# Kernel tuning notes

Measured on AMD Instinct MI355X. Metric: run time of the kernel, lower is better.

Reference implementation:

```python
import jax, jax.numpy as jnp
import numpy as np

B, L, D, H = 2, 2048, 1024, 16
DK = D // H
EPS = 1e-6


def setup_inputs() -> dict:
    key = jax.random.key(0)
    ks = jax.random.split(key, 8)
    s = 0.02
    return {
        "key": jax.random.normal(ks[0], (B, L, D), jnp.float32),
        "value": jax.random.normal(ks[1], (B, L, D), jnp.float32),
        "query": jax.random.normal(ks[2], (B, L, D), jnp.float32),
        "mask": jax.random.randint(ks[3], (B, L, L), 0, 2).astype(bool),
        "W_k": jax.random.normal(ks[4], (D, D), jnp.float32) * s,
        "W_v": jax.random.normal(ks[5], (D, D), jnp.float32) * s,
        "W_q": jax.random.normal(ks[6], (D, D), jnp.float32) * s,
        "ln_g": jnp.ones((D,), jnp.float32),
        "ln_b": jnp.zeros((D,), jnp.float32),
    }


def _mha(key, value, query, mask, W_k, W_v, W_q, ln_g, ln_b):
    b, l, d = key.shape
    # projections (bias=False), split into heads: [b, h, l, dk]
    def proj(x, W):
        return (x @ W).reshape(b, -1, H, DK).transpose(0, 2, 1, 3)
    k_up, v_up, q_up = proj(key, W_k), proj(value, W_v), proj(query, W_q)
    # scores [b, h, q, k]
    scores = jnp.einsum("bhqd,bhkd->bhqk", q_up, k_up) / jnp.sqrt(jnp.asarray(DK, scores_dtype(q_up)))
    scores = jnp.where(mask[:, None, :, :], -1e9, scores)
    attn = jax.nn.softmax(scores, axis=-1)  # dropout = identity (eval mode)
    out = jnp.einsum("bhqk,bhkd->bhqd", attn, v_up)
    out = out.transpose(0, 2, 1, 3).reshape(b, -1, d)
    res = out + query  # res_dropout = identity
    mu = jnp.mean(res, axis=-1, keepdims=True)
    var = jnp.var(res, axis=-1, keepdims=True)
    normed = (res - mu) * jax.lax.rsqrt(var + EPS) * ln_g + ln_b
    return normed, attn.reshape(b * H, attn.shape[2], attn.shape[3])


def scores_dtype(x):
    return x.dtype


def reference(key, value, query, mask, W_k, W_v, W_q, ln_g, ln_b):
    return _mha(key, value, query, mask, W_k, W_v, W_q, ln_g, ln_b)
```

## Files before the change

### kernel.cpp

```cpp
#include <hip/hip_runtime.h>
#include <math.h>

#define BATCH 2
#define SEQ   2048
#define DMODEL 1024
#define NHEAD 16
#define DK    64
#define EPS   1e-6f

typedef unsigned short ushort_t;
typedef __attribute__((ext_vector_type(8))) __bf16 bf16x8;
typedef __attribute__((ext_vector_type(4))) float f32x4;
typedef __attribute__((ext_vector_type(4))) unsigned int uivec4;

union B8U { uivec4 u; bf16x8 v; };

__device__ __forceinline__ ushort_t f2b(float x) {
    union { float f; unsigned int u; } c; c.f = x;
    unsigned int r = (c.u + 0x7fffu + ((c.u >> 16) & 1u)) >> 16;
    return (ushort_t)r;
}
__device__ __forceinline__ float b2f(ushort_t b) {
    union { unsigned int u; float f; } c; c.u = ((unsigned int)b) << 16;
    return c.f;
}
__device__ __forceinline__ bf16x8 ld_frag_lds(const ushort_t* p) {
    B8U t; t.u = *reinterpret_cast<const uivec4*>(p); return t.v;
}
__device__ __forceinline__ bf16x8 ld_frag_glb(const ushort_t* p) {
    B8U t; t.u = *reinterpret_cast<const uivec4*>(p); return t.v;
}
#define MFMA16(a, b, c) __builtin_amdgcn_mfma_f32_16x16x32_bf16((a), (b), (c), 0, 0, 0)

__global__ __launch_bounds__(256) void mask_to_bits(const int* __restrict__ mask,
                                                    unsigned int* __restrict__ bits) {
    const size_t widx = (size_t)blockIdx.x * 256 + threadIdx.x;
    const int4* src = reinterpret_cast<const int4*>(mask + widx * 32);
    unsigned int wv = 0;
    #pragma unroll
    for (int i = 0; i < 8; ++i) {
        int4 v = src[i];
        wv |= (v.x ? 1u : 0u) << (i * 4 + 0);
        wv |= (v.y ? 1u : 0u) << (i * 4 + 1);
        wv |= (v.z ? 1u : 0u) << (i * 4 + 2);
        wv |= (v.w ? 1u : 0u) << (i * 4 + 3);
    }
    bits[widx] = wv;
}

#define AST 40
#define BST 40
__global__ __launch_bounds__(256) void gemm_proj3(const float* __restrict__ X0,
                                                  const float* __restrict__ X1,
                                                  const float* __restrict__ X2,
                                                  const float* __restrict__ W0,
                                                  const float* __restrict__ W1,
                                                  const float* __restrict__ W2,
                                                  ushort_t* __restrict__ Y0,
                                                  ushort_t* __restrict__ Y1,
                                                  ushort_t* __restrict__ Y2) {
    __shared__ __align__(16) ushort_t As[128 * AST];
    __shared__ __align__(16) ushort_t Bt[128 * BST];
    const int z = blockIdx.z;
    const float* X = (z == 0) ? X0 : (z == 1) ? X1 : X2;
    const float* W = (z == 0) ? W0 : (z == 1) ? W1 : W2;
    ushort_t*    Y = (z == 0) ? Y0 : (z == 1) ? Y1 : Y2;

    const int t = threadIdx.x;
    const int bm = blockIdx.y * 128;
    const int bn = blockIdx.x * 128;
    const int w = t >> 6, lane = t & 63;
    const int ln16 = lane & 15, quad = lane >> 4;
    const int wr = w >> 1, wc = w & 1;

    f32x4 acc[4][4] = {};

    for (int k0 = 0; k0 < DMODEL; k0 += 32) {
        {
            const int m = t >> 1, half = t & 1;
            const float* src = X + (size_t)(bm + m) * DMODEL + k0 + half * 16;
            ushort_t* dst = &As[m * AST + half * 16];
            #pragma unroll
            for (int i = 0; i < 16; ++i) dst[i] = f2b(src[i]);
        }
        {
            const int kk = t >> 3, n0 = (t & 7) * 16;
            const float* src = W + (size_t)(k0 + kk) * DMODEL + bn + n0;
            #pragma unroll
            for (int i = 0; i < 16; ++i) Bt[(n0 + i) * BST + kk] = f2b(src[i]);
        }
        __syncthreads();
        bf16x8 af[4], bfr[4];
        #pragma unroll
        for (int rt = 0; rt < 4; ++rt)
            af[rt] = ld_frag_lds(&As[(wr * 64 + rt * 16 + ln16) * AST + quad * 8]);
        #pragma unroll
        for (int ct = 0; ct < 4; ++ct)
            bfr[ct] = ld_frag_lds(&Bt[(wc * 64 + ct * 16 + ln16) * BST + quad * 8]);
        #pragma unroll
        for (int rt = 0; rt < 4; ++rt)
            #pragma unroll
            for (int ct = 0; ct < 4; ++ct)
                acc[rt][ct] = MFMA16(af[rt], bfr[ct], acc[rt][ct]);
        __syncthreads();
    }
    #pragma unroll
    for (int rt = 0; rt < 4; ++rt) {
        #pragma unroll
        for (int ct = 0; ct < 4; ++ct) {
            #pragma unroll
            for (int r = 0; r < 4; ++r) {
                int row = bm + wr * 64 + rt * 16 + quad * 4 + r;
                int col = bn + wc * 64 + ct * 16 + ln16;
                Y[(size_t)row * DMODEL + col] = f2b(acc[rt][ct][r]);
            }
        }
    }
}

__global__ __launch_bounds__(256) void transpose_v(const ushort_t* __restrict__ v_up,
                                                   ushort_t* __restrict__ v_t) {
    __shared__ ushort_t tile[64][68];
    const int t = threadIdx.x;
    const int s0 = blockIdx.x * 64;
    const int bh = blockIdx.y;
    const int b = bh >> 4, h = bh & 15;
    {
        const int r = t >> 2, c0 = (t & 3) * 16;
        const ushort_t* src = v_up + ((size_t)b * SEQ + s0 + r) * DMODEL + h * DK + c0;
        #pragma unroll
        for (int i = 0; i < 16; ++i) tile[r][c0 + i] = src[i];
    }
    __syncthreads();
    {
        const int c = t >> 2, r0 = (t & 3) * 16;
        ushort_t* dst = v_t + ((size_t)bh * DK + c) * SEQ + s0 + r0;
        #pragma unroll
        for (int i = 0; i < 16; ++i) dst[i] = tile[r0 + i][c];
    }
}

#define PST 264
__global__ __launch_bounds__(512, 4) void attn_fused(const ushort_t* __restrict__ q_up,
                                                     const ushort_t* __restrict__ k_up,
                                                     const ushort_t* __restrict__ v_t,
                                                     const unsigned int* __restrict__ mbits,
                                                     float* __restrict__ attn,
                                                     float* __restrict__ o_ws) {
    __shared__ __align__(16) ushort_t Pb[32 * PST];
    __shared__ float psum[8][32];
    __shared__ float inv_s[32];

    const int t = threadIdx.x;
    const int w = t >> 6, lane = t & 63;
    const int ln16 = lane & 15, quad = lane >> 4;
    const int q0 = blockIdx.x * 32;
    const int bh = blockIdx.y;
    const int b = bh >> 4, h = bh & 15;

    bf16x8 aq[2][2];
    #pragma unroll
    for (int rt = 0; rt < 2; ++rt)
        #pragma unroll
        for (int ks = 0; ks < 2; ++ks)
            aq[rt][ks] = ld_frag_glb(
                &q_up[((size_t)b * SEQ + q0 + rt * 16 + ln16) * DMODEL + h * DK + ks * 32 + quad * 8]);

    const unsigned int* mrow = mbits + ((size_t)b * SEQ + q0) * (SEQ / 32);
    const ushort_t* kbase = &k_up[(size_t)b * SEQ * DMODEL + h * DK + quad * 8];

    float rs[2][4] = {};
    for (int i = 0; i < 16; ++i) {
        const int kt = (i * 8 + w) * 16;
        bf16x8 bk0 = ld_frag_glb(kbase + (size_t)(kt + ln16) * DMODEL);
        bf16x8 bk1 = ld_frag_glb(kbase + (size_t)(kt + ln16) * DMODEL + 32);
        const int wi = kt >> 5;
        const int bsh = (kt & 16) + ln16;
        #pragma unroll
        for (int rt = 0; rt < 2; ++rt) {
            f32x4 c = {0.f, 0.f, 0.f, 0.f};
            c = MFMA16(aq[rt][0], bk0, c);
            c = MFMA16(aq[rt][1], bk1, c);
            #pragma unroll
            for (int r = 0; r < 4; ++r) {
                const int row = rt * 16 + quad * 4 + r;
                const unsigned int mw = mrow[(size_t)row * (SEQ / 32) + wi];
                const float p = ((mw >> bsh) & 1u) ? 0.f : __expf(c[r] * 0.125f);
                rs[rt][r] += p;
            }
        }
    }
    #pragma unroll
    for (int rt = 0; rt < 2; ++rt)
        #pragma unroll
        for (int r = 0; r < 4; ++r) {
            float v = rs[rt][r];
            v += __shfl_xor(v, 1);
            v += __shfl_xor(v, 2);
            v += __shfl_xor(v, 4);
            v += __shfl_xor(v, 8);
            rs[rt][r] = v;
        }
    if (ln16 == 0) {
        #pragma unroll
        for (int rt = 0; rt < 2; ++rt)
            #pragma unroll
            for (int r = 0; r < 4; ++r)
                psum[w][rt * 16 + quad * 4 + r] = rs[rt][r];
    }
    __syncthreads();
    if (t < 32) {
        float s = 0.f;
        #pragma unroll
        for (int j = 0; j < 8; ++j) s += psum[j][t];
        inv_s[t] = 1.f / s;
    }
    __syncthreads();
    float invr[2][4];
    #pragma unroll
    for (int rt = 0; rt < 2; ++rt)
        #pragma unroll
        for (int r = 0; r < 4; ++r)
            invr[rt][r] = inv_s[rt * 16 + quad * 4 + r];

    const int prt = w >> 2, pct = w & 3;
    f32x4 acc = {0.f, 0.f, 0.f, 0.f};
    const ushort_t* vbase = &v_t[((size_t)bh * DK + pct * 16 + ln16) * SEQ + quad * 8];
    float* abase = attn + ((size_t)bh * SEQ + q0) * SEQ;
    const ushort_t* prow = &Pb[(prt * 16 + ln16) * PST + quad * 8];

    for (int kb = 0; kb < SEQ; kb += 256) {
        #pragma unroll
        for (int tl = 0; tl < 2; ++tl) {
            const int kt = kb + (w * 2 + tl) * 16;
            bf16x8 bk0 = ld_frag_glb(kbase + (size_t)(kt + ln16) * DMODEL);
            bf16x8 bk1 = ld_frag_glb(kbase + (size_t)(kt + ln16) * DMODEL + 32);
            const int wi = kt >> 5;
            const int bsh = (kt & 16) + ln16;
            #pragma unroll
            for (int rt = 0; rt < 2; ++rt) {
                f32x4 c = {0.f, 0.f, 0.f, 0.f};
                c = MFMA16(aq[rt][0], bk0, c);
                c = MFMA16(aq[rt][1], bk1, c);
                #pragma unroll
                for (int r = 0; r < 4; ++r) {
                    const int row = rt * 16 + quad * 4 + r;
                    const unsigned int mw = mrow[(size_t)row * (SEQ / 32) + wi];
                    const float p = ((mw >> bsh) & 1u) ? 0.f : __expf(c[r] * 0.125f);
                    const float pn = p * invr[rt][r];
                    __builtin_nontemporal_store(pn, &abase[(size_t)row * SEQ + kt + ln16]);
                    Pb[row * PST + (kt - kb) + ln16] = f2b(pn);
                }
            }
        }
        __syncthreads();
        #pragma unroll
        for (int k0 = 0; k0 < 256; k0 += 32) {
            bf16x8 a  = ld_frag_lds(prow + k0);
            bf16x8 vb = ld_frag_glb(vbase + kb + k0);
            acc = MFMA16(a, vb, acc);
        }
        __syncthreads();
    }
    #pragma unroll
    for (int r = 0; r < 4; ++r) {
        const int row = q0 + prt * 16 + quad * 4 + r;
        const int col = h * DK + pct * 16 + ln16;
        o_ws[((size_t)b * SEQ + row) * DMODEL + col] = acc[r];
    }
}

__global__ __launch_bounds__(256) void ln_kernel(const float* __restrict__ O,
                                                 const float* __restrict__ Qin,
                                                 const float* __restrict__ g,
                                                 const float* __restrict__ bt,
                                                 float* __restrict__ out) {
    __shared__ float sm[256];
    const int tid = threadIdx.x;
    const size_t base = (size_t)blockIdx.x * DMODEL;
    float v[4];
    float s = 0.f, s2 = 0.f;
    #pragma unroll
    for (int i = 0; i < 4; ++i) {
        int d = tid + i * 256;
        float x = O[base + d] + Qin[base + d];
        v[i] = x;
        s += x;
        s2 += x * x;
    }
    sm[tid] = s; __syncthreads();
    for (int st = 128; st > 0; st >>= 1) {
        if (tid < st) sm[tid] += sm[tid + st];
        __syncthreads();
    }
    s = sm[0]; __syncthreads();
    sm[tid] = s2; __syncthreads();
    for (int st = 128; st > 0; st >>= 1) {
        if (tid < st) sm[tid] += sm[tid + st];
        __syncthreads();
    }
    s2 = sm[0];
    const float mu = s * (1.0f / DMODEL);
    const float var = s2 * (1.0f / DMODEL) - mu * mu;
    const float r = rsqrtf(var + EPS);
    #pragma unroll
    for (int i = 0; i < 4; ++i) {
        int d = tid + i * 256;
        out[base + d] = (v[i] - mu) * r * g[d] + bt[d];
    }
}

extern "C" void kernel_launch(void* const* d_in, const int* in_sizes, int n_in,
                              void* d_out, int out_size, void* d_ws, size_t ws_size,
                              hipStream_t stream) {
    const float* key   = (const float*)d_in[0];
    const float* value = (const float*)d_in[1];
    const float* query = (const float*)d_in[2];
    const int*   mask  = (const int*)  d_in[3];
    const float* W_k   = (const float*)d_in[4];
    const float* W_v   = (const float*)d_in[5];
    const float* W_q   = (const float*)d_in[6];
    const float* ln_g  = (const float*)d_in[7];
    const float* ln_b  = (const float*)d_in[8];

    float* out      = (float*)d_out;
    float* attn_out = out + (size_t)BATCH * SEQ * DMODEL;

    const size_t NPROJ = (size_t)BATCH * SEQ * DMODEL;
    ushort_t* k_up = (ushort_t*)d_ws;
    ushort_t* v_up = k_up + NPROJ;
    ushort_t* q_up = v_up + NPROJ;
    ushort_t* v_t  = q_up + NPROJ;
    float*    o_ws = (float*)(v_t + NPROJ);
    unsigned int* mbits = (unsigned int*)(o_ws + NPROJ);

    const int nwords = BATCH * SEQ * (SEQ / 32);
    mask_to_bits<<<nwords / 256, 256, 0, stream>>>(mask, mbits);

    dim3 gproj(DMODEL / 128, (BATCH * SEQ) / 128, 3);
    gemm_proj3<<<gproj, 256, 0, stream>>>(key, value, query, W_k, W_v, W_q, k_up, v_up, q_up);

    dim3 gtr(SEQ / 64, BATCH * NHEAD);
    transpose_v<<<gtr, 256, 0, stream>>>(v_up, v_t);

    dim3 gat(SEQ / 32, BATCH * NHEAD);
    attn_fused<<<gat, 512, 0, stream>>>(q_up, k_up, v_t, mbits, attn_out, o_ws);

    ln_kernel<<<BATCH * SEQ, 256, 0, stream>>>(o_ws, query, ln_g, ln_b, out);
}
```

Before: 919.5 us.

## Pre-convert inputs and weights to bf16, load GEMM tiles via global_load_lds

Adds separate kernels that convert the three fp32 activations to bf16 and transpose-convert the weights to bf16 N-major. The projection GEMM then streams tiles straight into LDS with global_load_lds instead of per-element fp32 loads, conversion and strided transposed LDS stores. It also raises wave priority around MFMA sections in the GEMM and attention kernels. In exchange it adds extra kernel launches, more workspace traffic, and an unpadded LDS layout that may cause bank conflicts.

```diff
diff --git a/kernel.cpp b/kernel.cpp
--- a/kernel.cpp
+++ b/kernel.cpp
@@ -30,6 +30,12 @@
 __device__ __forceinline__ bf16x8 ld_frag_glb(const ushort_t* p) {
     B8U t; t.u = *reinterpret_cast<const uivec4*>(p); return t.v;
 }
+__device__ __forceinline__ void gload_lds16(const ushort_t* g, ushort_t* l) {
+    __builtin_amdgcn_global_load_lds(
+        (const __attribute__((address_space(1))) unsigned int*)g,
+        (__attribute__((address_space(3))) unsigned int*)l,
+        16, 0, 0);
+}
 #define MFMA16(a, b, c) __builtin_amdgcn_mfma_f32_16x16x32_bf16((a), (b), (c), 0, 0, 0)
 
 __global__ __launch_bounds__(256) void mask_to_bits(const int* __restrict__ mask,
@@ -48,23 +54,67 @@
     bits[widx] = wv;
 }
 
-#define AST 40
-#define BST 40
-__global__ __launch_bounds__(256) void gemm_proj3(const float* __restrict__ X0,
+__global__ __launch_bounds__(256) void cvt_bf16x3(const float* __restrict__ X0,
                                                   const float* __restrict__ X1,
                                                   const float* __restrict__ X2,
-                                                  const float* __restrict__ W0,
-                                                  const float* __restrict__ W1,
-                                                  const float* __restrict__ W2,
                                                   ushort_t* __restrict__ Y0,
                                                   ushort_t* __restrict__ Y1,
                                                   ushort_t* __restrict__ Y2) {
-    __shared__ __align__(16) ushort_t As[128 * AST];
-    __shared__ __align__(16) ushort_t Bt[128 * BST];
+    const int z = blockIdx.y;
+    const float* X = (z == 0) ? X0 : (z == 1) ? X1 : X2;
+    ushort_t*    Y = (z == 0) ? Y0 : (z == 1) ? Y1 : Y2;
+    const size_t i = ((size_t)blockIdx.x * 256 + threadIdx.x) * 8;
+    float4 a = *reinterpret_cast<const float4*>(X + i);
+    float4 b = *reinterpret_cast<const float4*>(X + i + 4);
+    ushort_t o[8];
+    o[0] = f2b(a.x); o[1] = f2b(a.y); o[2] = f2b(a.z); o[3] = f2b(a.w);
+    o[4] = f2b(b.x); o[5] = f2b(b.y); o[6] = f2b(b.z); o[7] = f2b(b.w);
+    *reinterpret_cast<uivec4*>(Y + i) = *reinterpret_cast<const uivec4*>(o);
+}
+
+__global__ __launch_bounds__(256) void transpose_w3(const float* __restrict__ W0,
+                                                    const float* __restrict__ W1,
+                                                    const float* __restrict__ W2,
+                                                    ushort_t* __restrict__ T0,
+                                                    ushort_t* __restrict__ T1,
+                                                    ushort_t* __restrict__ T2) {
+    __shared__ ushort_t tile[64][68];
     const int z = blockIdx.z;
-    const float* X = (z == 0) ? X0 : (z == 1) ? X1 : X2;
     const float* W = (z == 0) ? W0 : (z == 1) ? W1 : W2;
-    ushort_t*    Y = (z == 0) ? Y0 : (z == 1) ? Y1 : Y2;
+    ushort_t*    T = (z == 0) ? T0 : (z == 1) ? T1 : T2;
+    const int k0 = blockIdx.x * 64;
+    const int n0 = blockIdx.y * 64;
+    const int t = threadIdx.x;
+    {
+        const int r = t >> 2, c0 = (t & 3) * 16;
+        const float* src = W + (size_t)(k0 + r) * DMODEL + n0 + c0;
+        #pragma unroll
+        for (int i = 0; i < 16; ++i) tile[r][c0 + i] = f2b(src[i]);
+    }
+    __syncthreads();
+    {
+        const int c = t >> 2, r0 = (t & 3) * 16;
+        ushort_t* dst = T + (size_t)(n0 + c) * DMODEL + k0 + r0;
+        #pragma unroll
+        for (int i = 0; i < 16; ++i) dst[i] = tile[r0 + i][c];
+    }
+}
+
+__global__ __launch_bounds__(256) void gemm_proj3(const ushort_t* __restrict__ Xb0,
+                                                  const ushort_t* __restrict__ Xb1,
+                                                  const ushort_t* __restrict__ Xb2,
+                                                  const ushort_t* __restrict__ Wt0,
+                                                  const ushort_t* __restrict__ Wt1,
+                                                  const ushort_t* __restrict__ Wt2,
+                                                  ushort_t* __restrict__ Y0,
+                                                  ushort_t* __restrict__ Y1,
+                                                  ushort_t* __restrict__ Y2) {
+    __shared__ __align__(16) ushort_t As[128 * 32];
+    __shared__ __align__(16) ushort_t Bs[128 * 32];
+    const int z = blockIdx.z;
+    const ushort_t* Xb = (z == 0) ? Xb0 : (z == 1) ? Xb1 : Xb2;
+    const ushort_t* Wt = (z == 0) ? Wt0 : (z == 1) ? Wt1 : Wt2;
+    ushort_t*       Y  = (z == 0) ? Y0  : (z == 1) ? Y1  : Y2;
 
     const int t = threadIdx.x;
     const int bm = blockIdx.y * 128;
@@ -73,35 +123,34 @@
     const int ln16 = lane & 15, quad = lane >> 4;
     const int wr = w >> 1, wc = w & 1;
 
+    const int srow = lane >> 2;
+    const int selem = (lane & 3) * 8;
+
     f32x4 acc[4][4] = {};
 
     for (int k0 = 0; k0 < DMODEL; k0 += 32) {
-        {
-            const int m = t >> 1, half = t & 1;
-            const float* src = X + (size_t)(bm + m) * DMODEL + k0 + half * 16;
-            ushort_t* dst = &As[m * AST + half * 16];
-            #pragma unroll
-            for (int i = 0; i < 16; ++i) dst[i] = f2b(src[i]);
-        }
-        {
-            const int kk = t >> 3, n0 = (t & 7) * 16;
-            const float* src = W + (size_t)(k0 + kk) * DMODEL + bn + n0;
-            #pragma unroll
-            for (int i = 0; i < 16; ++i) Bt[(n0 + i) * BST + kk] = f2b(src[i]);
+        #pragma unroll
+        for (int j = 0; j < 2; ++j) {
+            const int g = w * 2 + j;
+            const int m = g * 16 + srow;
+            gload_lds16(Xb + (size_t)(bm + m) * DMODEL + k0 + selem, &As[g * 512]);
+            gload_lds16(Wt + (size_t)(bn + m) * DMODEL + k0 + selem, &Bs[g * 512]);
         }
         __syncthreads();
         bf16x8 af[4], bfr[4];
         #pragma unroll
         for (int rt = 0; rt < 4; ++rt)
-            af[rt] = ld_frag_lds(&As[(wr * 64 + rt * 16 + ln16) * AST + quad * 8]);
+            af[rt] = ld_frag_lds(&As[(wr * 64 + rt * 16 + ln16) * 32 + quad * 8]);
         #pragma unroll
         for (int ct = 0; ct < 4; ++ct)
-            bfr[ct] = ld_frag_lds(&Bt[(wc * 64 + ct * 16 + ln16) * BST + quad * 8]);
+            bfr[ct] = ld_frag_lds(&Bs[(wc * 64 + ct * 16 + ln16) * 32 + quad * 8]);
+        __builtin_amdgcn_s_setprio(1);
         #pragma unroll
         for (int rt = 0; rt < 4; ++rt)
             #pragma unroll
             for (int ct = 0; ct < 4; ++ct)
                 acc[rt][ct] = MFMA16(af[rt], bfr[ct], acc[rt][ct]);
+        __builtin_amdgcn_s_setprio(0);
         __syncthreads();
     }
     #pragma unroll
@@ -179,8 +228,10 @@
         #pragma unroll
         for (int rt = 0; rt < 2; ++rt) {
             f32x4 c = {0.f, 0.f, 0.f, 0.f};
+            __builtin_amdgcn_s_setprio(1);
             c = MFMA16(aq[rt][0], bk0, c);
             c = MFMA16(aq[rt][1], bk1, c);
+            __builtin_amdgcn_s_setprio(0);
             #pragma unroll
             for (int r = 0; r < 4; ++r) {
                 const int row = rt * 16 + quad * 4 + r;
@@ -240,8 +291,10 @@
             #pragma unroll
             for (int rt = 0; rt < 2; ++rt) {
                 f32x4 c = {0.f, 0.f, 0.f, 0.f};
+                __builtin_amdgcn_s_setprio(1);
                 c = MFMA16(aq[rt][0], bk0, c);
                 c = MFMA16(aq[rt][1], bk1, c);
+                __builtin_amdgcn_s_setprio(0);
                 #pragma unroll
                 for (int r = 0; r < 4; ++r) {
                     const int row = rt * 16 + quad * 4 + r;
@@ -254,12 +307,14 @@
             }
         }
         __syncthreads();
+        __builtin_amdgcn_s_setprio(1);
         #pragma unroll
         for (int k0 = 0; k0 < 256; k0 += 32) {
             bf16x8 a  = ld_frag_lds(prow + k0);
             bf16x8 vb = ld_frag_glb(vbase + kb + k0);
             acc = MFMA16(a, vb, acc);
         }
+        __builtin_amdgcn_s_setprio(0);
         __syncthreads();
     }
     #pragma unroll
@@ -327,18 +382,31 @@
     float* attn_out = out + (size_t)BATCH * SEQ * DMODEL;
 
     const size_t NPROJ = (size_t)BATCH * SEQ * DMODEL;
+    const size_t NW    = (size_t)DMODEL * DMODEL;
     ushort_t* k_up = (ushort_t*)d_ws;
     ushort_t* v_up = k_up + NPROJ;
     ushort_t* q_up = v_up + NPROJ;
     ushort_t* v_t  = q_up + NPROJ;
-    float*    o_ws = (float*)(v_t + NPROJ);
+    ushort_t* kb   = v_t + NPROJ;
+    ushort_t* vb   = kb + NPROJ;
+    ushort_t* qb   = vb + NPROJ;
+    ushort_t* wtk  = qb + NPROJ;
+    ushort_t* wtv  = wtk + NW;
+    ushort_t* wtq  = wtv + NW;
+    float*    o_ws = (float*)(wtq + NW);
     unsigned int* mbits = (unsigned int*)(o_ws + NPROJ);
 
     const int nwords = BATCH * SEQ * (SEQ / 32);
     mask_to_bits<<<nwords / 256, 256, 0, stream>>>(mask, mbits);
 
+    dim3 gcvt((unsigned)(NPROJ / (256 * 8)), 3);
+    cvt_bf16x3<<<gcvt, 256, 0, stream>>>(key, value, query, kb, vb, qb);
+
+    dim3 gtw(DMODEL / 64, DMODEL / 64, 3);
+    transpose_w3<<<gtw, 256, 0, stream>>>(W_k, W_v, W_q, wtk, wtv, wtq);
+
     dim3 gproj(DMODEL / 128, (BATCH * SEQ) / 128, 3);
-    gemm_proj3<<<gproj, 256, 0, stream>>>(key, value, query, W_k, W_v, W_q, k_up, v_up, q_up);
+    gemm_proj3<<<gproj, 256, 0, stream>>>(kb, vb, qb, wtk, wtv, wtq, k_up, v_up, q_up);
 
     dim3 gtr(SEQ / 64, BATCH * NHEAD);
     transpose_v<<<gtr, 256, 0, stream>>>(v_up, v_t);
```

Result: no change. 931.7 us (+1.3%).
